# Kernel tuning notes

Hardware: AMD Instinct MI355X
Metric: run time of the kernel (lower is better)

## Reference

```python
import jax, jax.numpy as jnp
import numpy as np

LATENT_DIM = 128
KQ_DIM = 32
B, N, K = 4, 16384, 64


def setup_inputs() -> dict:
    key = jax.random.key(0)
    k1, k2, k3, k4, k5, k6, k7 = jax.random.split(key, 7)
    return {
        "indices": jax.random.randint(k1, (3, B, N, K), 0, N, dtype=jnp.int64)
        if jax.config.jax_enable_x64 else jax.random.randint(k1, (3, B, N, K), 0, N, dtype=jnp.int32),
        "img": jax.random.normal(k2, (B, 3, 128, 128), dtype=jnp.float32),
        "features": jax.random.normal(k3, (B, N, LATENT_DIM), dtype=jnp.float32),
        "Wk": jax.random.normal(k4, (KQ_DIM, LATENT_DIM), dtype=jnp.float32) * 0.05,
        "bk": jax.random.normal(k5, (KQ_DIM,), dtype=jnp.float32) * 0.05,
        "Wq": jax.random.normal(k6, (KQ_DIM, LATENT_DIM), dtype=jnp.float32) * 0.05,
        "bq": jax.random.normal(k7, (KQ_DIM,), dtype=jnp.float32) * 0.05,
    }


def reference(indices, img, features, Wk, bk, Wq, bq):
    # features: [B, N, latent] -> keys/queries: [B, N, D]
    ks = jnp.einsum("bnl,dl->bnd", features, Wk) + bk
    qs = jnp.einsum("bnl,dl->bnd", features, Wq) + bq
    D = ks.shape[-1]
    # indices row 1 indexes keys, row 2 indexes queries (values in [0, N))
    x_idx = indices[1].reshape(B, N * K)  # [B, N*K]
    y_idx = indices[2].reshape(B, N * K)
    # gather along node axis: [B, N*K, D]
    x_feat = jnp.take_along_axis(ks, x_idx[:, :, None], axis=1)
    y_feat = jnp.take_along_axis(qs, y_idx[:, :, None], axis=1)
    # scaled dot product per edge -> [B, N, K]
    logits = (x_feat * y_feat).sum(axis=-1).reshape(B, N, K) * (D ** -0.5)
    return logits
```

## Files before the change

### kernel.cpp

```cpp
#include <hip/hip_runtime.h>
#include <hip/hip_fp16.h>

#define LATENT 128
#define DQK    32
#define BB     4
#define NN     16384
#define KK     64
#define TOTAL_EDGES (BB * NN * KK)
#define TOTAL_NODES (BB * NN)
#define PAD    132
#define EG     8

typedef _Float16 half8 __attribute__((ext_vector_type(8)));
typedef float    f32x4 __attribute__((ext_vector_type(4)));

__global__ __launch_bounds__(256, 2) void proj_kernel(
    const float* __restrict__ features,
    const float* __restrict__ Wk,
    const float* __restrict__ bk,
    const float* __restrict__ Wq,
    const float* __restrict__ bq,
    __half* __restrict__ ks,
    __half* __restrict__ qs)
{
    __shared__ float sf[64 * PAD];
    __shared__ float sw[64 * PAD];
    __shared__ float sb[64];

    const int t = threadIdx.x;
    const int node0 = blockIdx.x * 64;

    #pragma unroll
    for (int j = 0; j < 8; ++j) {
        int idx = t + j * 256;
        int r = idx >> 5;
        int c = idx & 31;
        const float4* src = (r < 32) ? (const float4*)Wk : (const float4*)Wq;
        float4 v = src[(size_t)(r & 31) * 32 + c];
        *(float4*)&sw[r * PAD + c * 4] = v;
    }
    if (t < 64) sb[t] = (t < 32) ? bk[t] : bq[t - 32];

    #pragma unroll
    for (int j = 0; j < 8; ++j) {
        int idx = t + j * 256;
        int r = idx >> 5;
        int c = idx & 31;
        float4 v = ((const float4*)(features + (size_t)(node0 + r) * LATENT))[c];
        *(float4*)&sf[r * PAD + c * 4] = v;
    }
    __syncthreads();

    const int tx = t & 15;
    const int ty = t >> 4;

    float acc[4][4];
    #pragma unroll
    for (int i = 0; i < 4; ++i)
        #pragma unroll
        for (int u = 0; u < 4; ++u) acc[i][u] = 0.f;

    #pragma unroll 4
    for (int kk = 0; kk < 32; ++kk) {
        float4 a[4], b[4];
        #pragma unroll
        for (int i = 0; i < 4; ++i)
            a[i] = *(const float4*)&sf[(ty * 4 + i) * PAD + kk * 4];
        #pragma unroll
        for (int u = 0; u < 4; ++u)
            b[u] = *(const float4*)&sw[(tx + 16 * u) * PAD + kk * 4];
        #pragma unroll
        for (int i = 0; i < 4; ++i)
            #pragma unroll
            for (int u = 0; u < 4; ++u)
                acc[i][u] += a[i].x * b[u].x + a[i].y * b[u].y
                           + a[i].z * b[u].z + a[i].w * b[u].w;
    }

    #pragma unroll
    for (int u = 0; u < 4; ++u) {
        const int d = tx + 16 * u;
        const float bias = sb[d];
        __half* base = (d < 32) ? ks : qs;
        const int dd = d & 31;
        #pragma unroll
        for (int i = 0; i < 4; ++i) {
            const int node = node0 + ty * 4 + i;
            base[(size_t)node * DQK + dd] = __float2half(acc[i][u] + bias);
        }
    }
}

__global__ __launch_bounds__(256, 2) void edge_kernel(
    const int* __restrict__ xidx,
    const int* __restrict__ yidx,
    const __half* __restrict__ ks,
    const __half* __restrict__ qs,
    float* __restrict__ out)
{
    const int lane = threadIdx.x & 63;
    const int wave = (blockIdx.x * 256 + threadIdx.x) >> 6;
    const int i = lane & 15;
    const int c = lane >> 4;
    const int e_base = wave * (16 * EG);
    const int b = e_base >> 20;
    const int nodebase = b << 14;

    const _Float16* ksh = (const _Float16*)ks;
    const _Float16* qsh = (const _Float16*)qs;

    int xs[EG], ys[EG];
    #pragma unroll
    for (int g = 0; g < EG; ++g) {
        xs[g] = xidx[e_base + g * 16 + i];
        ys[g] = yidx[e_base + g * 16 + i];
    }
    __builtin_amdgcn_sched_barrier(0);

    half8 kv[EG], qv[EG];
    #pragma unroll
    for (int g = 0; g < EG; ++g) {
        kv[g] = *(const half8*)(ksh + (((size_t)(nodebase + xs[g])) << 5) + (c << 3));
        qv[g] = *(const half8*)(qsh + (((size_t)(nodebase + ys[g])) << 5) + (c << 3));
    }
    __builtin_amdgcn_sched_barrier(0);

    const bool writer = (c == (i >> 2));
    const int reg = i & 3;
    #pragma unroll
    for (int g = 0; g < EG; ++g) {
        f32x4 acc = {0.f, 0.f, 0.f, 0.f};
        acc = __builtin_amdgcn_mfma_f32_16x16x32_f16(kv[g], qv[g], acc, 0, 0, 0);
        float v = acc[0];
        v = (reg == 1) ? acc[1] : v;
        v = (reg == 2) ? acc[2] : v;
        v = (reg == 3) ? acc[3] : v;
        if (writer) out[e_base + g * 16 + i] = v * 0.17677669529663687f;
    }
}

extern "C" void kernel_launch(void* const* d_in, const int* in_sizes, int n_in,
                              void* d_out, int out_size, void* d_ws, size_t ws_size,
                              hipStream_t stream) {
    const int*   indices  = (const int*)d_in[0];
    const float* features = (const float*)d_in[2];
    const float* Wk       = (const float*)d_in[3];
    const float* bk       = (const float*)d_in[4];
    const float* Wq       = (const float*)d_in[5];
    const float* bq       = (const float*)d_in[6];
    float* out = (float*)d_out;

    __half* ks = (__half*)d_ws;
    __half* qs = ks + (size_t)TOTAL_NODES * DQK;

    const int* xidx = indices + (size_t)1 * TOTAL_EDGES;
    const int* yidx = indices + (size_t)2 * TOTAL_EDGES;

    proj_kernel<<<TOTAL_NODES / 64, 256, 0, stream>>>(features, Wk, bk, Wq, bq, ks, qs);
    edge_kernel<<<TOTAL_EDGES / 512, 256, 0, stream>>>(xidx, yidx, ks, qs, out);
}
```

Measured before the change: 77.65 us.

## Pipeline per-batch projection with previous batch's edge gather in staged launches

Merges the projection and edge kernels into one stage kernel launched five times. Each launch projects batch s while computing edges for batch s-1, so the two kinds of work overlap on the GPU. It also stores the weights in LDS as fp16 to shrink shared memory. The cost is more launches and the tail stages, and the fp16 weight rounding adds a small numerical change.

```diff
diff --git a/kernel.cpp b/kernel.cpp
--- a/kernel.cpp
+++ b/kernel.cpp
@@ -8,134 +8,143 @@
 #define KK     64
 #define TOTAL_EDGES (BB * NN * KK)
 #define TOTAL_NODES (BB * NN)
-#define PAD    132
+#define EPB     (NN * KK)
+#define PADF   132
+#define PADH   136
 #define EG     8
+#define EDGE_BLOCKS 2048
+#define PROJ_BLOCKS 256
 
 typedef _Float16 half8 __attribute__((ext_vector_type(8)));
 typedef float    f32x4 __attribute__((ext_vector_type(4)));
 
-__global__ __launch_bounds__(256, 2) void proj_kernel(
+__global__ __launch_bounds__(256, 2) void stage_kernel(
     const float* __restrict__ features,
     const float* __restrict__ Wk,
     const float* __restrict__ bk,
     const float* __restrict__ Wq,
     const float* __restrict__ bq,
+    const int* __restrict__ xidx,
+    const int* __restrict__ yidx,
     __half* __restrict__ ks,
-    __half* __restrict__ qs)
+    __half* __restrict__ qs,
+    float* __restrict__ out,
+    int eb, int pb, int nProj)
 {
-    __shared__ float sf[64 * PAD];
-    __shared__ float sw[64 * PAD];
-    __shared__ float sb[64];
+    __shared__ float  sf[64 * PADF];
+    __shared__ __half swh[64 * PADH];
+    __shared__ float  sb[64];
 
     const int t = threadIdx.x;
-    const int node0 = blockIdx.x * 64;
 
-    #pragma unroll
-    for (int j = 0; j < 8; ++j) {
-        int idx = t + j * 256;
-        int r = idx >> 5;
-        int c = idx & 31;
-        const float4* src = (r < 32) ? (const float4*)Wk : (const float4*)Wq;
-        float4 v = src[(size_t)(r & 31) * 32 + c];
-        *(float4*)&sw[r * PAD + c * 4] = v;
-    }
-    if (t < 64) sb[t] = (t < 32) ? bk[t] : bq[t - 32];
+    if ((int)blockIdx.x < nProj) {
+        const int node0 = (pb << 14) + blockIdx.x * 64;
 
-    #pragma unroll
-    for (int j = 0; j < 8; ++j) {
-        int idx = t + j * 256;
-        int r = idx >> 5;
-        int c = idx & 31;
-        float4 v = ((const float4*)(features + (size_t)(node0 + r) * LATENT))[c];
-        *(float4*)&sf[r * PAD + c * 4] = v;
-    }
-    __syncthreads();
+        #pragma unroll
+        for (int j = 0; j < 8; ++j) {
+            int idx = t + j * 256;
+            int r = idx >> 5;
+            int c = idx & 31;
+            const float4* src = (r < 32) ? (const float4*)Wk : (const float4*)Wq;
+            float4 v = src[(size_t)(r & 31) * 32 + c];
+            *(__half2*)&swh[r * PADH + c * 4]     = __floats2half2_rn(v.x, v.y);
+            *(__half2*)&swh[r * PADH + c * 4 + 2] = __floats2half2_rn(v.z, v.w);
+        }
+        if (t < 64) sb[t] = (t < 32) ? bk[t] : bq[t - 32];
 
-    const int tx = t & 15;
-    const int ty = t >> 4;
+        #pragma unroll
+        for (int j = 0; j < 8; ++j) {
+            int idx = t + j * 256;
+            int r = idx >> 5;
+            int c = idx & 31;
+            float4 v = ((const float4*)(features + (size_t)(node0 + r) * LATENT))[c];
+            *(float4*)&sf[r * PADF + c * 4] = v;
+        }
+        __syncthreads();
 
-    float acc[4][4];
-    #pragma unroll
-    for (int i = 0; i < 4; ++i)
-        #pragma unroll
-        for (int u = 0; u < 4; ++u) acc[i][u] = 0.f;
+        const int tx = t & 15;
+        const int ty = t >> 4;
 
-    #pragma unroll 4
-    for (int kk = 0; kk < 32; ++kk) {
-        float4 a[4], b[4];
-        #pragma unroll
-        for (int i = 0; i < 4; ++i)
-            a[i] = *(const float4*)&sf[(ty * 4 + i) * PAD + kk * 4];
-        #pragma unroll
-        for (int u = 0; u < 4; ++u)
-            b[u] = *(const float4*)&sw[(tx + 16 * u) * PAD + kk * 4];
+        float acc[4][4];
         #pragma unroll
         for (int i = 0; i < 4; ++i)
             #pragma unroll
-            for (int u = 0; u < 4; ++u)
-                acc[i][u] += a[i].x * b[u].x + a[i].y * b[u].y
-                           + a[i].z * b[u].z + a[i].w * b[u].w;
-    }
+            for (int u = 0; u < 4; ++u) acc[i][u] = 0.f;
 
-    #pragma unroll
-    for (int u = 0; u < 4; ++u) {
-        const int d = tx + 16 * u;
-        const float bias = sb[d];
-        __half* base = (d < 32) ? ks : qs;
-        const int dd = d & 31;
+        #pragma unroll 4
+        for (int kk = 0; kk < 32; ++kk) {
+            float4 a[4];
+            #pragma unroll
+            for (int i = 0; i < 4; ++i)
+                a[i] = *(const float4*)&sf[(ty * 4 + i) * PADF + kk * 4];
+            float4 b[4];
+            #pragma unroll
+            for (int u = 0; u < 4; ++u) {
+                const int row = tx + 16 * u;
+                float2 f01 = __half22float2(*(const __half2*)&swh[row * PADH + kk * 4]);
+                float2 f23 = __half22float2(*(const __half2*)&swh[row * PADH + kk * 4 + 2]);
+                b[u] = make_float4(f01.x, f01.y, f23.x, f23.y);
+            }
+            #pragma unroll
+            for (int i = 0; i < 4; ++i)
+                #pragma unroll
+                for (int u = 0; u < 4; ++u)
+                    acc[i][u] += a[i].x * b[u].x + a[i].y * b[u].y
+                               + a[i].z * b[u].z + a[i].w * b[u].w;
+        }
+
         #pragma unroll
-        for (int i = 0; i < 4; ++i) {
-            const int node = node0 + ty * 4 + i;
-            base[(size_t)node * DQK + dd] = __float2half(acc[i][u] + bias);
+        for (int u = 0; u < 4; ++u) {
+            const int d = tx + 16 * u;
+            const float bias = sb[d];
+            __half* base = (d < 32) ? ks : qs;
+            const int dd = d & 31;
+            #pragma unroll
+            for (int i = 0; i < 4; ++i) {
+                const int node = node0 + ty * 4 + i;
+                base[(size_t)node * DQK + dd] = __float2half(acc[i][u] + bias);
+            }
         }
-    }
-}
+    } else {
+        const int ebid = blockIdx.x - nProj;
+        const int lane = t & 63;
+        const int wave = (ebid * 256 + t) >> 6;
+        const int i = lane & 15;
+        const int c = lane >> 4;
+        const int e_base = (eb << 20) + wave * (16 * EG);
+        const int nodebase = eb << 14;
 
-__global__ __launch_bounds__(256, 2) void edge_kernel(
-    const int* __restrict__ xidx,
-    const int* __restrict__ yidx,
-    const __half* __restrict__ ks,
-    const __half* __restrict__ qs,
-    float* __restrict__ out)
-{
-    const int lane = threadIdx.x & 63;
-    const int wave = (blockIdx.x * 256 + threadIdx.x) >> 6;
-    const int i = lane & 15;
-    const int c = lane >> 4;
-    const int e_base = wave * (16 * EG);
-    const int b = e_base >> 20;
-    const int nodebase = b << 14;
+        const _Float16* ksh = (const _Float16*)ks;
+        const _Float16* qsh = (const _Float16*)qs;
 
-    const _Float16* ksh = (const _Float16*)ks;
-    const _Float16* qsh = (const _Float16*)qs;
+        int xs[EG], ys[EG];
+        #pragma unroll
+        for (int g = 0; g < EG; ++g) {
+            xs[g] = xidx[e_base + g * 16 + i];
+            ys[g] = yidx[e_base + g * 16 + i];
+        }
+        __builtin_amdgcn_sched_barrier(0);
 
-    int xs[EG], ys[EG];
-    #pragma unroll
-    for (int g = 0; g < EG; ++g) {
-        xs[g] = xidx[e_base + g * 16 + i];
-        ys[g] = yidx[e_base + g * 16 + i];
-    }
-    __builtin_amdgcn_sched_barrier(0);
+        half8 kv[EG], qv[EG];
+        #pragma unroll
+        for (int g = 0; g < EG; ++g) {
+            kv[g] = *(const half8*)(ksh + (((size_t)(nodebase + xs[g])) << 5) + (c << 3));
+            qv[g] = *(const half8*)(qsh + (((size_t)(nodebase + ys[g])) << 5) + (c << 3));
+        }
+        __builtin_amdgcn_sched_barrier(0);
 
-    half8 kv[EG], qv[EG];
-    #pragma unroll
-    for (int g = 0; g < EG; ++g) {
-        kv[g] = *(const half8*)(ksh + (((size_t)(nodebase + xs[g])) << 5) + (c << 3));
-        qv[g] = *(const half8*)(qsh + (((size_t)(nodebase + ys[g])) << 5) + (c << 3));
-    }
-    __builtin_amdgcn_sched_barrier(0);
-
-    const bool writer = (c == (i >> 2));
-    const int reg = i & 3;
-    #pragma unroll
-    for (int g = 0; g < EG; ++g) {
-        f32x4 acc = {0.f, 0.f, 0.f, 0.f};
-        acc = __builtin_amdgcn_mfma_f32_16x16x32_f16(kv[g], qv[g], acc, 0, 0, 0);
-        float v = acc[0];
-        v = (reg == 1) ? acc[1] : v;
-        v = (reg == 2) ? acc[2] : v;
-        v = (reg == 3) ? acc[3] : v;
-        if (writer) out[e_base + g * 16 + i] = v * 0.17677669529663687f;
+        const bool writer = (c == (i >> 2));
+        const int reg = i & 3;
+        #pragma unroll
+        for (int g = 0; g < EG; ++g) {
+            f32x4 acc = {0.f, 0.f, 0.f, 0.f};
+            acc = __builtin_amdgcn_mfma_f32_16x16x32_f16(kv[g], qv[g], acc, 0, 0, 0);
+            float v = acc[0];
+            v = (reg == 1) ? acc[1] : v;
+            v = (reg == 2) ? acc[2] : v;
+            v = (reg == 3) ? acc[3] : v;
+            if (writer) out[e_base + g * 16 + i] = v * 0.17677669529663687f;
+        }
     }
 }
 
@@ -156,6 +165,12 @@
     const int* xidx = indices + (size_t)1 * TOTAL_EDGES;
     const int* yidx = indices + (size_t)2 * TOTAL_EDGES;
 
-    proj_kernel<<<TOTAL_NODES / 64, 256, 0, stream>>>(features, Wk, bk, Wq, bq, ks, qs);
-    edge_kernel<<<TOTAL_EDGES / 512, 256, 0, stream>>>(xidx, yidx, ks, qs, out);
+    for (int s = 0; s < 5; ++s) {
+        const int eb = s - 1;
+        const int pb = s;
+        const int nProj = (pb < BB) ? PROJ_BLOCKS : 0;
+        const int nEdge = (eb >= 0) ? EDGE_BLOCKS : 0;
+        stage_kernel<<<nProj + nEdge, 256, 0, stream>>>(
+            features, Wk, bk, Wq, bq, xidx, yidx, ks, qs, out, eb, pb, nProj);
+    }
 }
```

After: 79.51 us. 2.4% more time.
